# Performance work log

Measured on AMD Instinct MI355X. Metric: run time of the kernel, lower is better.

Reference implementation:

```python
import jax, jax.numpy as jnp
import numpy as np

WINDOWP = 64
LN_EPS = 1e-5


def setup_inputs() -> dict:
    key = jax.random.key(0)
    ks = jax.random.split(key, 4)
    B, T, D = 8, 2048, 1024
    feature = jax.random.normal(ks[0], (B, T, D), dtype=jnp.float32)
    wq_w = jax.random.normal(ks[1], (D, D), dtype=jnp.float32) * 0.02  # x @ wq_w + wq_b
    wq_b = jnp.zeros((D,), dtype=jnp.float32)
    w2_w = jax.random.normal(ks[2], (D,), dtype=jnp.float32) * 0.02
    w2_b = jnp.zeros((1,), dtype=jnp.float32)
    ln_g = jnp.ones((D,), dtype=jnp.float32)
    ln_b = jnp.zeros((D,), dtype=jnp.float32)
    return {"feature": feature, "wq_w": wq_w, "wq_b": wq_b,
            "w2_w": w2_w, "w2_b": w2_b, "ln_g": ln_g, "ln_b": ln_b}


def _layer_norm(y, g, b):
    mu = jnp.mean(y, axis=-1, keepdims=True)
    var = jnp.mean((y - mu) ** 2, axis=-1, keepdims=True)
    return (y - mu) * jax.lax.rsqrt(var + LN_EPS) * g + b


def reference(feature, wq_w, wq_b, w2_w, w2_b, ln_g, ln_b):
    # feature: [B, T, D]
    B, T, D = feature.shape
    W = WINDOWP
    q_local = feature @ wq_w + wq_b  # [B, T, D]

    # First W positions: v_local[:, i] = feature[:, i]
    init_buf = feature[:, :W, :]  # sliding buffer of last W outputs, [B, W, D]

    def step(buf, q_i):
        # ki = v_local[:, i-W : i+1]; slot i is still zero when read (torch writes after)
        ki = jnp.concatenate([buf, jnp.zeros((B, 1, D), feature.dtype)], axis=1)  # [B, W+1, D]
        scores = jnp.einsum('bwd,d->bw', q_i[:, None, :] * ki, w2_w) + w2_b[0]  # [B, W+1]
        alpha = jax.nn.softmax(scores, axis=1)
        v_i = jnp.einsum('bwd,bw->bd', ki, alpha)  # [B, D]
        new_buf = jnp.concatenate([buf[:, 1:, :], v_i[:, None, :]], axis=1)
        return new_buf, v_i

    qs = jnp.transpose(q_local[:, W:, :], (1, 0, 2))  # [T-W, B, D]
    _, vs = jax.lax.scan(step, init_buf, qs)          # vs: [T-W, B, D]
    v_local = jnp.concatenate([feature[:, :W, :], jnp.transpose(vs, (1, 0, 2))], axis=1)

    y = jnp.tanh(v_local) * feature + feature
    return _layer_norm(y, ln_g, ln_b)
```

## Files before the change

### kernel.cpp

```cpp
#include <hip/hip_runtime.h>
#include <hip/hip_bf16.h>

#define B_ 8
#define T_ 2048
#define D_ 1024
#define W_ 64
#define LN_EPS 1e-5f
#define LOG2E 1.4426950408889634f

typedef __attribute__((ext_vector_type(8))) short bf16x8;
typedef __attribute__((ext_vector_type(4))) float f32x4;
typedef __attribute__((ext_vector_type(2))) float f32x2;
typedef unsigned short ushort_t;

__device__ __forceinline__ ushort_t f32_to_bf16(float f) {
    union { float ff; unsigned u; } c; c.ff = f;
    unsigned r = (c.u + 0x7fffu + ((c.u >> 16) & 1u)) >> 16;
    return (ushort_t)r;
}
__device__ __forceinline__ float bf16_to_f32(ushort_t h) {
    union { unsigned u; float f; } c; c.u = ((unsigned)h) << 16; return c.f;
}
__device__ __forceinline__ float tanh_fast(float x) {
    float xx = fminf(fmaxf(x, -20.f), 20.f);
    float e = __expf(2.f * xx);
    return 1.f - 2.f / (e + 1.f);
}
__device__ __forceinline__ float readlane_f(float v, int l) {
    return __int_as_float(__builtin_amdgcn_readlane(__float_as_int(v), l));
}
template <int CTRL>
__device__ __forceinline__ float dpp_add(float x) {
    int y = __builtin_amdgcn_update_dpp(0, __float_as_int(x), CTRL, 0xf, 0xf, true);
    return x + __int_as_float(y);
}
template <int CTRL>
__device__ __forceinline__ f32x2 pk_dpp_add(f32x2 v) {
    f32x2 t;
    t.x = __int_as_float(__builtin_amdgcn_update_dpp(0, __float_as_int(v.x), CTRL, 0xf, 0xf, true));
    t.y = __int_as_float(__builtin_amdgcn_update_dpp(0, __float_as_int(v.y), CTRL, 0xf, 0xf, true));
    return v + t;
}
__device__ __forceinline__ f32x2 sum64_pair(f32x2 v) {
    v = pk_dpp_add<0x111>(v);
    v = pk_dpp_add<0x112>(v);
    v = pk_dpp_add<0x114>(v);
    v = pk_dpp_add<0x118>(v);
    v = pk_dpp_add<0x142>(v);
    v = pk_dpp_add<0x143>(v);
    return v;
}
__device__ __forceinline__ f32x2 lo2(f32x4 v) { return __builtin_shufflevector(v, v, 0, 1); }
__device__ __forceinline__ f32x2 hi2(f32x4 v) { return __builtin_shufflevector(v, v, 2, 3); }

__global__ void cvt_feat(const float* __restrict__ f, ushort_t* __restrict__ o, int n) {
    int i = blockIdx.x * blockDim.x + threadIdx.x;
    if (i < n) o[i] = f32_to_bf16(f[i]);
}

__global__ void cvt_wqT(const float* __restrict__ wq, ushort_t* __restrict__ o) {
    __shared__ float tile[64][65];
    int bi = blockIdx.x, bj = blockIdx.y, tid = threadIdx.x;
    int c = tid & 63, r4 = tid >> 6;
    for (int it = 0; it < 16; ++it) {
        int r = it * 4 + r4;
        tile[r][c] = wq[(size_t)(bi * 64 + r) * D_ + bj * 64 + c];
    }
    __syncthreads();
    for (int it = 0; it < 16; ++it) {
        int r = it * 4 + r4;
        o[(size_t)(bj * 64 + r) * D_ + bi * 64 + c] = f32_to_bf16(tile[c][r]);
    }
}

__global__ __launch_bounds__(256) void gemm_qw(
        const ushort_t* __restrict__ A, const ushort_t* __restrict__ BT,
        const float* __restrict__ wqb, const float* __restrict__ w2w,
        float* __restrict__ out) {
    const int K = 1024;
    __shared__ ushort_t Al[128][48];
    __shared__ ushort_t Bl[64][48];
    int tid = threadIdx.x;
    int lane = tid & 63, wv = tid >> 6;
    int wm = wv >> 1, wn = wv & 1;
    int m0 = blockIdx.x * 128, n0 = blockIdx.y * 64;
    int mrow = lane & 15, quad = lane >> 4;
    f32x4 acc[4][2] = {};
    for (int k0 = 0; k0 < K; k0 += 32) {
#pragma unroll
        for (int rep = 0; rep < 2; ++rep) {
            int idx = rep * 256 + tid;
            int r = idx >> 2, cp = (idx & 3) * 8;
            *(bf16x8*)&Al[r][cp] = *(const bf16x8*)&A[(size_t)(m0 + r) * K + k0 + cp];
        }
        {
            int r = tid >> 2, cp = (tid & 3) * 8;
            *(bf16x8*)&Bl[r][cp] = *(const bf16x8*)&BT[(size_t)(n0 + r) * K + k0 + cp];
        }
        __syncthreads();
        bf16x8 af[4], bfr[2];
#pragma unroll
        for (int ms = 0; ms < 4; ++ms) af[ms] = *(bf16x8*)&Al[wm * 64 + ms * 16 + mrow][quad * 8];
#pragma unroll
        for (int ns = 0; ns < 2; ++ns) bfr[ns] = *(bf16x8*)&Bl[wn * 32 + ns * 16 + mrow][quad * 8];
#pragma unroll
        for (int ms = 0; ms < 4; ++ms)
#pragma unroll
            for (int ns = 0; ns < 2; ++ns)
                acc[ms][ns] = __builtin_amdgcn_mfma_f32_16x16x32_bf16(af[ms], bfr[ns], acc[ms][ns], 0, 0, 0);
        __syncthreads();
    }
#pragma unroll
    for (int ns = 0; ns < 2; ++ns) {
        int n = n0 + wn * 32 + ns * 16 + mrow;
        float scale = w2w[n] * LOG2E, bias = wqb[n];
#pragma unroll
        for (int ms = 0; ms < 4; ++ms) {
#pragma unroll
            for (int r = 0; r < 4; ++r) {
                int m = m0 + wm * 64 + ms * 16 + quad * 4 + r;
                out[(size_t)m * D_ + n] = (acc[ms][ns][r] + bias) * scale;
            }
        }
    }
}

__global__ void featT_kernel(const float* __restrict__ feat, float* __restrict__ fT32,
                             ushort_t* __restrict__ fTh, ushort_t* __restrict__ fTl) {
    __shared__ float tile[64][65];
    int d0 = blockIdx.x * 64, b = blockIdx.y, tid = threadIdx.x;
    int c = tid & 63, r4 = tid >> 6;
#pragma unroll
    for (int it = 0; it < 16; ++it) {
        int r = it * 4 + r4;
        tile[r][c] = feat[((size_t)b * T_ + r) * D_ + d0 + c];
    }
    __syncthreads();
#pragma unroll
    for (int it = 0; it < 16; ++it) {
        int r = it * 4 + r4;
        float v = tile[c][r];
        size_t o = ((size_t)b * D_ + d0 + r) * 64 + c;
        fT32[o] = v;
        ushort_t h = f32_to_bf16(v);
        fTh[o] = h;
        fTl[o] = f32_to_bf16(v - bf16_to_f32(h));
    }
}

__global__ __launch_bounds__(256) void s0_gemm(
        const float* __restrict__ qw, const float* __restrict__ fT32,
        ushort_t* __restrict__ S0h, ushort_t* __restrict__ S0l) {
    __shared__ float As[64][17];
    __shared__ float Bs[16][65];
    int b = blockIdx.y;
    int t0 = 64 + blockIdx.x * 64;
    int tx = threadIdx.x & 15, ty = threadIdx.x >> 4;
    float acc[4][4] = {};
    for (int k0 = 0; k0 < D_; k0 += 16) {
#pragma unroll
        for (int i = 0; i < 4; ++i) {
            int idx = i * 256 + threadIdx.x;
            int r = idx >> 4, c = idx & 15;
            As[r][c] = qw[((size_t)b * T_ + t0 + r) * D_ + k0 + c];
        }
#pragma unroll
        for (int i = 0; i < 4; ++i) {
            int idx = i * 256 + threadIdx.x;
            int r = idx >> 6, c = idx & 63;
            Bs[r][c] = fT32[((size_t)b * D_ + k0 + r) * 64 + c];
        }
        __syncthreads();
#pragma unroll
        for (int kk = 0; kk < 16; ++kk)
#pragma unroll
            for (int i = 0; i < 4; ++i)
#pragma unroll
                for (int j = 0; j < 4; ++j)
                    acc[i][j] = fmaf(As[ty * 4 + i][kk], Bs[kk][tx * 4 + j], acc[i][j]);
        __syncthreads();
    }
#pragma unroll
    for (int i = 0; i < 4; ++i)
#pragma unroll
        for (int j = 0; j < 4; ++j) {
            float sc = acc[i][j];
            ushort_t h = f32_to_bf16(sc);
            size_t o = ((size_t)b * T_ + t0 + ty * 4 + i) * 64 + tx * 4 + j;
            S0h[o] = h;
            S0l[o] = f32_to_bf16(sc - bf16_to_f32(h));
        }
}

__global__ __launch_bounds__(64, 1) void core_kernel(
        const ushort_t* __restrict__ S0h, const ushort_t* __restrict__ S0l,
        float* __restrict__ gamma) {
    const int b = blockIdx.x;
    const int lane = threadIdx.x;
    const int n16 = lane & 15, quad = lane >> 4;
    __shared__ float ULDS[64 * 67];
    __shared__ __align__(16) float ALPH[64 * 68];
    __shared__ __align__(16) float B1L[16 * 68];
    __shared__ ushort_t CH[64 * 72];
    __shared__ ushort_t CL[64 * 72];
    __shared__ ushort_t CWTh[64 * 72];
    __shared__ ushort_t CWTl[64 * 72];

#pragma unroll
    for (int jj = 0; jj < 72; ++jj) {
        ushort_t idv = (jj == lane) ? (ushort_t)0x3F80 : (ushort_t)0;
        CH[lane * 72 + jj] = idv;  CL[lane * 72 + jj] = 0;
        CWTh[lane * 72 + jj] = idv; CWTl[lane * 72 + jj] = 0;
    }

#pragma unroll 1
    for (int p = 0; p < 31; ++p) {
        const int t0 = 64 + (p << 6);

        {
            bf16x8 Bh[4][2], Blo[4][2];
#pragma unroll
            for (int nt = 0; nt < 4; ++nt)
#pragma unroll
                for (int kt = 0; kt < 2; ++kt) {
                    int a = (nt * 16 + n16) * 72 + kt * 32 + quad * 8;
                    Bh[nt][kt] = *(const bf16x8*)&CH[a];
                    Blo[nt][kt] = *(const bf16x8*)&CL[a];
                }
#pragma unroll
            for (int mt = 0; mt < 4; ++mt) {
                bf16x8 Ah[2], Alo2[2];
#pragma unroll
                for (int kt = 0; kt < 2; ++kt) {
                    size_t a = ((size_t)b * T_ + t0 + mt * 16 + n16) * 64 + kt * 32 + quad * 8;
                    Ah[kt] = *(const bf16x8*)&S0h[a];
                    Alo2[kt] = *(const bf16x8*)&S0l[a];
                }
                f32x4 acc[4] = {};
#pragma unroll
                for (int nt = 0; nt < 4; ++nt)
#pragma unroll
                    for (int kt = 0; kt < 2; ++kt) {
                        acc[nt] = __builtin_amdgcn_mfma_f32_16x16x32_bf16(Ah[kt], Bh[nt][kt], acc[nt], 0, 0, 0);
                        acc[nt] = __builtin_amdgcn_mfma_f32_16x16x32_bf16(Ah[kt], Blo[nt][kt], acc[nt], 0, 0, 0);
                        acc[nt] = __builtin_amdgcn_mfma_f32_16x16x32_bf16(Alo2[kt], Bh[nt][kt], acc[nt], 0, 0, 0);
                    }
#pragma unroll
                for (int nt = 0; nt < 4; ++nt)
#pragma unroll
                    for (int r = 0; r < 4; ++r)
                        ULDS[(mt * 16 + quad * 4 + r) * 67 + nt * 16 + n16] = acc[nt][r];
            }
        }

        f32x2 Xa2[8], Xb2[8], Xc2[8], Xd2[8];
#pragma unroll
        for (int l2 = 0; l2 < 8; ++l2) {
            Xa2[l2].x = ULDS[lane * 67 + 2 * l2];
            Xa2[l2].y = ULDS[lane * 67 + 2 * l2 + 1];
            Xb2[l2].x = ULDS[lane * 67 + 16 + 2 * l2];
            Xb2[l2].y = ULDS[lane * 67 + 16 + 2 * l2 + 1];
            Xc2[l2].x = ULDS[lane * 67 + 32 + 2 * l2];
            Xc2[l2].y = ULDS[lane * 67 + 32 + 2 * l2 + 1];
            Xd2[l2].x = ULDS[lane * 67 + 48 + 2 * l2];
            Xd2[l2].y = ULDS[lane * 67 + 48 + 2 * l2 + 1];
        }
        float row = ULDS[lane];
        float nxt = ULDS[67 + lane];

#pragma unroll 1
        for (int j = 0; j < 4; ++j) {
#pragma unroll
            for (int sl = 0; sl < 16; ++sl) {
                const int s = (j << 4) | sl;
                const bool c61 = (sl <= 13);
                const bool c63 = (sl <= 14);
                bool do61 = c61 || (j < 3);
                bool do63 = c63 || (j < 3);
                float e = __builtin_amdgcn_exp2f(row);
                ALPH[s * 68 + lane] = e;
                f32x4 A[16];
                if (do63) {
#pragma unroll
                    for (int i = 0; i < 16; ++i)
                        A[i] = *(const f32x4*)&ALPH[s * 68 + i * 4];
                }
                float nxt2v = 0.f;
                if (do61) nxt2v = ULDS[(s + 2) * 67 + lane];
                f32x2 v; v.x = e; v.y = e * nxt;
                v = sum64_pair(v);
                float tot = readlane_f(v.x, 63) + 1.f;
                float cs  = readlane_f(v.y, 63);
                float r = __builtin_amdgcn_rcpf(tot);
                if (do63) {
                    float u_next = cs * r;
                    f32x2 acc0 = {0.f, 0.f}, acc1 = {0.f, 0.f}, acc2 = {0.f, 0.f}, acc3 = {0.f, 0.f};
#pragma unroll
                    for (int i2 = 0; i2 < 4; ++i2) {
                        f32x4 aa = A[i2];
                        acc0 = __builtin_elementwise_fma(lo2(aa), Xa2[2 * i2], acc0);
                        acc1 = __builtin_elementwise_fma(hi2(aa), Xa2[2 * i2 + 1], acc1);
                        f32x4 ab = A[4 + i2];
                        acc2 = __builtin_elementwise_fma(lo2(ab), Xb2[2 * i2], acc2);
                        acc3 = __builtin_elementwise_fma(hi2(ab), Xb2[2 * i2 + 1], acc3);
                        f32x4 ac = A[8 + i2];
                        acc0 = __builtin_elementwise_fma(lo2(ac), Xc2[2 * i2], acc0);
                        acc1 = __builtin_elementwise_fma(hi2(ac), Xc2[2 * i2 + 1], acc1);
                        f32x4 ad = A[12 + i2];
                        acc2 = __builtin_elementwise_fma(lo2(ad), Xd2[2 * i2], acc2);
                        acc3 = __builtin_elementwise_fma(hi2(ad), Xd2[2 * i2 + 1], acc3);
                    }
                    f32x2 u2 = (acc0 + acc1) + (acc2 + acc3);
                    float u_new = (u2.x + u2.y) * r;
                    if (j == 0)      { if (sl & 1) Xa2[sl >> 1].y = u_new; else Xa2[sl >> 1].x = u_new; }
                    else if (j == 1) { if (sl & 1) Xb2[sl >> 1].y = u_new; else Xb2[sl >> 1].x = u_new; }
                    else if (j == 2) { if (sl & 1) Xc2[sl >> 1].y = u_new; else Xc2[sl >> 1].x = u_new; }
                    else             { if (sl & 1) Xd2[sl >> 1].y = u_new; else Xd2[sl >> 1].x = u_new; }
                    if (lane > s) ULDS[lane * 67 + s] = u_new;
                    row = (lane == s) ? u_next : nxt;
                    if (do61) {
                        float pu = readlane_f(u_new, s + 2);
                        nxt = (lane == s) ? pu : nxt2v;
                    } else {
                        nxt = 0.f;
                    }
                }
                if (lane == 0) ALPH[s * 68 + 64] = r;
            }

            {
                const int J0 = j << 4;
                float rrow = ALPH[(J0 + n16) * 68 + 64];
                bf16x8 Aah[2], Aal[2];
#pragma unroll
                for (int kt = 0; kt < 2; ++kt) {
                    float v[8];
                    *(float4*)&v[0] = *(const float4*)&ALPH[(J0 + n16) * 68 + kt * 32 + quad * 8];
                    *(float4*)&v[4] = *(const float4*)&ALPH[(J0 + n16) * 68 + kt * 32 + quad * 8 + 4];
                    bf16x8 h, l;
#pragma unroll
                    for (int i = 0; i < 8; ++i) {
                        float val = v[i] * rrow;
                        ushort_t hh = f32_to_bf16(val);
                        h[i] = (short)hh;
                        l[i] = (short)f32_to_bf16(val - bf16_to_f32(hh));
                    }
                    Aah[kt] = h; Aal[kt] = l;
                }
#pragma unroll
                for (int nt = 0; nt < 4; ++nt) {
                    f32x4 a = {};
#pragma unroll
                    for (int kt = 0; kt < 2; ++kt) {
                        bf16x8 bh = *(const bf16x8*)&CWTh[(nt * 16 + n16) * 72 + kt * 32 + quad * 8];
                        bf16x8 bl = *(const bf16x8*)&CWTl[(nt * 16 + n16) * 72 + kt * 32 + quad * 8];
                        a = __builtin_amdgcn_mfma_f32_16x16x32_bf16(Aah[kt], bh, a, 0, 0, 0);
                        a = __builtin_amdgcn_mfma_f32_16x16x32_bf16(Aah[kt], bl, a, 0, 0, 0);
                        a = __builtin_amdgcn_mfma_f32_16x16x32_bf16(Aal[kt], bh, a, 0, 0, 0);
                    }
#pragma unroll
                    for (int r = 0; r < 4; ++r)
                        B1L[(quad * 4 + r) * 68 + nt * 16 + n16] = a[r];
                }
                float D[16];
#pragma unroll
                for (int sl = 0; sl < 16; ++sl) {
                    float corr = 0.f;
                    const float* arow = &ALPH[(J0 + sl) * 68 + J0];
#pragma unroll
                    for (int c = 0; c < 4; ++c) {
                        if (sl > 4 * c) {
                            float4 am = *(const float4*)&arow[4 * c];
                            if (sl > 4 * c + 0) corr = fmaf(am.x, D[4 * c + 0], corr);
                            if (sl > 4 * c + 1) corr = fmaf(am.y, D[4 * c + 1], corr);
                            if (sl > 4 * c + 2) corr = fmaf(am.z, D[4 * c + 2], corr);
                            if (sl > 4 * c + 3) corr = fmaf(am.w, D[4 * c + 3], corr);
                        }
                    }
                    float rsl = ALPH[(J0 + sl) * 68 + 64];
                    float g = fmaf(rsl, corr, B1L[sl * 68 + lane]);
                    const int slot = J0 + sl;
                    float oldv = bf16_to_f32(CH[slot * 72 + lane]) + bf16_to_f32(CL[slot * 72 + lane]);
                    D[sl] = g - oldv;
                    gamma[((size_t)b * T_ + t0 + slot) * 64 + lane] = g;
                    ushort_t gh = f32_to_bf16(g);
                    ushort_t gl2 = f32_to_bf16(g - bf16_to_f32(gh));
                    CH[slot * 72 + lane] = gh;  CL[slot * 72 + lane] = gl2;
                    CWTh[lane * 72 + slot] = gh; CWTl[lane * 72 + slot] = gl2;
                }
            }
        }
    }
}

__global__ __launch_bounds__(256) void prologue_kernel(
        const float* __restrict__ feat, float* __restrict__ out,
        const float* __restrict__ lng, const float* __restrict__ lnb) {
    int b = blockIdx.y, t = blockIdx.x, tid = threadIdx.x;
    __shared__ float red[4][2];
    size_t base = ((size_t)b * T_ + t) * D_;
    float4 f4 = *(const float4*)&feat[base + tid * 4];
    float4 y;
    y.x = tanh_fast(f4.x) * f4.x + f4.x;
    y.y = tanh_fast(f4.y) * f4.y + f4.y;
    y.z = tanh_fast(f4.z) * f4.z + f4.z;
    y.w = tanh_fast(f4.w) * f4.w + f4.w;
    float s1 = y.x + y.y + y.z + y.w;
    float s2 = y.x * y.x + y.y * y.y + y.z * y.z + y.w * y.w;
#pragma unroll
    for (int m = 1; m < 64; m <<= 1) { s1 += __shfl_xor(s1, m, 64); s2 += __shfl_xor(s2, m, 64); }
    if ((tid & 63) == 0) { red[tid >> 6][0] = s1; red[tid >> 6][1] = s2; }
    __syncthreads();
    float mu = (red[0][0] + red[1][0] + red[2][0] + red[3][0]) * (1.f / D_);
    float m2 = (red[0][1] + red[1][1] + red[2][1] + red[3][1]) * (1.f / D_);
    float rv = rsqrtf(fmaxf(m2 - mu * mu, 0.f) + LN_EPS);
    float4 g4 = *(const float4*)&lng[tid * 4];
    float4 b4 = *(const float4*)&lnb[tid * 4];
    float4 o;
    o.x = (y.x - mu) * rv * g4.x + b4.x;
    o.y = (y.y - mu) * rv * g4.y + b4.y;
    o.z = (y.z - mu) * rv * g4.z + b4.z;
    o.w = (y.w - mu) * rv * g4.w + b4.w;
    *(float4*)&out[base + tid * 4] = o;
}

__global__ __launch_bounds__(256) void final_kernel(
        const float* __restrict__ gamma, const ushort_t* __restrict__ fTh,
        const ushort_t* __restrict__ fTl, const float* __restrict__ feat,
        const float* __restrict__ lng, const float* __restrict__ lnb,
        float* __restrict__ out) {
    const int b = blockIdx.y;
    const int t0 = 64 + blockIdx.x * 16;
    const int tid = threadIdx.x, lane = tid & 63, wv = tid >> 6;
    const int n16 = lane & 15, quad = lane >> 4;
    __shared__ float wsum[4][16][2];
    __shared__ float lnp[16][2];

    bf16x8 Ah[2], Alo[2];
    {
        const float* gr = &gamma[((size_t)b * T_ + t0 + n16) * 64];
#pragma unroll
        for (int kt = 0; kt < 2; ++kt) {
            float g[8];
            *(float4*)&g[0] = *(const float4*)&gr[kt * 32 + quad * 8];
            *(float4*)&g[4] = *(const float4*)&gr[kt * 32 + quad * 8 + 4];
            bf16x8 h, l;
#pragma unroll
            for (int i = 0; i < 8; ++i) {
                ushort_t hh = f32_to_bf16(g[i]);
                h[i] = (short)hh;
                l[i] = (short)f32_to_bf16(g[i] - bf16_to_f32(hh));
            }
            Ah[kt] = h; Alo[kt] = l;
        }
    }
    f32x4 acc[16];
#pragma unroll
    for (int j = 0; j < 16; ++j) {
        const int d = wv * 256 + j * 16 + n16;
        const ushort_t* fr = &fTh[((size_t)b * D_ + d) * 64];
        const ushort_t* fr2 = &fTl[((size_t)b * D_ + d) * 64];
        f32x4 a = {0.f, 0.f, 0.f, 0.f};
#pragma unroll
        for (int kt = 0; kt < 2; ++kt) {
            bf16x8 bh = *(const bf16x8*)&fr[kt * 32 + quad * 8];
            bf16x8 bl = *(const bf16x8*)&fr2[kt * 32 + quad * 8];
            a = __builtin_amdgcn_mfma_f32_16x16x32_bf16(Ah[kt], bh, a, 0, 0, 0);
            a = __builtin_amdgcn_mfma_f32_16x16x32_bf16(Ah[kt], bl, a, 0, 0, 0);
            a = __builtin_amdgcn_mfma_f32_16x16x32_bf16(Alo[kt], bh, a, 0, 0, 0);
        }
        acc[j] = a;
    }
    float s1[4] = {0.f, 0.f, 0.f, 0.f}, s2[4] = {0.f, 0.f, 0.f, 0.f};
#pragma unroll
    for (int j = 0; j < 16; ++j) {
        const int d = wv * 256 + j * 16 + n16;
#pragma unroll
        for (int r = 0; r < 4; ++r) {
            float f = feat[((size_t)b * T_ + t0 + quad * 4 + r) * D_ + d];
            float y = tanh_fast(acc[j][r]) * f + f;
            acc[j][r] = y;
            s1[r] += y;
            s2[r] += y * y;
        }
    }
#pragma unroll
    for (int m = 1; m < 16; m <<= 1)
#pragma unroll
        for (int r = 0; r < 4; ++r) { s1[r] += __shfl_xor(s1[r], m, 64); s2[r] += __shfl_xor(s2[r], m, 64); }
    if (n16 == 0) {
#pragma unroll
        for (int r = 0; r < 4; ++r) { wsum[wv][quad * 4 + r][0] = s1[r]; wsum[wv][quad * 4 + r][1] = s2[r]; }
    }
    __syncthreads();
    if (tid < 16) {
        float a = 0.f, c = 0.f;
#pragma unroll
        for (int w2 = 0; w2 < 4; ++w2) { a += wsum[w2][tid][0]; c += wsum[w2][tid][1]; }
        float mu = a * (1.f / D_);
        float var = c * (1.f / D_) - mu * mu;
        lnp[tid][0] = mu;
        lnp[tid][1] = rsqrtf(fmaxf(var, 0.f) + LN_EPS);
    }
    __syncthreads();
#pragma unroll
    for (int j = 0; j < 16; ++j) {
        const int d = wv * 256 + j * 16 + n16;
        float gd = lng[d], bd = lnb[d];
#pragma unroll
        for (int r = 0; r < 4; ++r) {
            int row = quad * 4 + r;
            out[((size_t)b * T_ + t0 + row) * D_ + d] = (acc[j][r] - lnp[row][0]) * lnp[row][1] * gd + bd;
        }
    }
}

extern "C" void kernel_launch(void* const* d_in, const int* in_sizes, int n_in,
                              void* d_out, int out_size, void* d_ws, size_t ws_size,
                              hipStream_t stream) {
    const float* feature = (const float*)d_in[0];
    const float* wq_w    = (const float*)d_in[1];
    const float* wq_b    = (const float*)d_in[2];
    const float* w2_w    = (const float*)d_in[3];
    const float* ln_g    = (const float*)d_in[5];
    const float* ln_b    = (const float*)d_in[6];
    float* out = (float*)d_out;

    uint8_t* ws = (uint8_t*)d_ws;
    ushort_t* featbf = (ushort_t*)(ws);
    ushort_t* wqT    = (ushort_t*)(ws + 32u * 1024 * 1024);
    float*    gamma = (float*)(ws);
    ushort_t* S0h   = (ushort_t*)(ws + 4u * 1024 * 1024);
    ushort_t* S0l   = (ushort_t*)(ws + 6u * 1024 * 1024);
    float*    fT32  = (float*)(ws + 8u * 1024 * 1024);
    ushort_t* fTh   = (ushort_t*)(ws + 10u * 1024 * 1024);
    ushort_t* fTl   = (ushort_t*)(ws + 11u * 1024 * 1024);

    const int ntot = B_ * T_ * D_;
    cvt_feat<<<(ntot + 255) / 256, 256, 0, stream>>>(feature, featbf, ntot);
    cvt_wqT<<<dim3(16, 16), 256, 0, stream>>>(wq_w, wqT);
    gemm_qw<<<dim3(128, 16), 256, 0, stream>>>(featbf, wqT, wq_b, w2_w, out);
    featT_kernel<<<dim3(16, 8), 256, 0, stream>>>(feature, fT32, fTh, fTl);
    s0_gemm<<<dim3(31, 8), 256, 0, stream>>>(out, fT32, S0h, S0l);
    core_kernel<<<8, 64, 0, stream>>>(S0h, S0l, gamma);
    prologue_kernel<<<dim3(64, 8), 256, 0, stream>>>(feature, out, ln_g, ln_b);
    final_kernel<<<dim3(124, 8), 256, 0, stream>>>(gamma, fTh, fTl, feature, ln_g, ln_b, out);
}
```

Before: 1.373 ms.

## Use split-bf16 MFMA for score GEMM and merge prep/prologue kernels

Replaces the fp32 FMA tiled s0_gemm with a three-product split-bf16 MFMA formulation that reads a new bf16 hi/lo copy of the first 64 feature rows produced in featT_kernel. Merges feature conversion and weight transpose into one launch, and folds the prologue LayerNorm blocks into final_kernel as extra blocks. Aims to cut the compute cost of the score GEMM and launch overhead, at the risk of slight precision change from the split-bf16 approximation.

After: 1.336 ms. 1.03x faster.

```diff
diff --git a/kernel.cpp b/kernel.cpp
--- a/kernel.cpp
+++ b/kernel.cpp
@@ -53,23 +53,30 @@
 __device__ __forceinline__ f32x2 lo2(f32x4 v) { return __builtin_shufflevector(v, v, 0, 1); }
 __device__ __forceinline__ f32x2 hi2(f32x4 v) { return __builtin_shufflevector(v, v, 2, 3); }
 
-__global__ void cvt_feat(const float* __restrict__ f, ushort_t* __restrict__ o, int n) {
-    int i = blockIdx.x * blockDim.x + threadIdx.x;
-    if (i < n) o[i] = f32_to_bf16(f[i]);
-}
-
-__global__ void cvt_wqT(const float* __restrict__ wq, ushort_t* __restrict__ o) {
+__global__ void prep_kernel(const float* __restrict__ f, ushort_t* __restrict__ o,
+                            const float* __restrict__ wq, ushort_t* __restrict__ wqT) {
     __shared__ float tile[64][65];
-    int bi = blockIdx.x, bj = blockIdx.y, tid = threadIdx.x;
-    int c = tid & 63, r4 = tid >> 6;
-    for (int it = 0; it < 16; ++it) {
-        int r = it * 4 + r4;
-        tile[r][c] = wq[(size_t)(bi * 64 + r) * D_ + bj * 64 + c];
-    }
-    __syncthreads();
-    for (int it = 0; it < 16; ++it) {
-        int r = it * 4 + r4;
-        o[(size_t)(bj * 64 + r) * D_ + bi * 64 + c] = f32_to_bf16(tile[c][r]);
+    int tid = threadIdx.x;
+    if (blockIdx.x < 32768) {
+        int i = blockIdx.x * 512 + tid * 2;
+        float2 v = *(const float2*)&f[i];
+        ushort2 w;
+        w.x = f32_to_bf16(v.x);
+        w.y = f32_to_bf16(v.y);
+        *(ushort2*)&o[i] = w;
+    } else {
+        int bid = blockIdx.x - 32768;
+        int bi = bid & 15, bj = bid >> 4;
+        int c = tid & 63, r4 = tid >> 6;
+        for (int it = 0; it < 16; ++it) {
+            int r = it * 4 + r4;
+            tile[r][c] = wq[(size_t)(bi * 64 + r) * D_ + bj * 64 + c];
+        }
+        __syncthreads();
+        for (int it = 0; it < 16; ++it) {
+            int r = it * 4 + r4;
+            wqT[(size_t)(bj * 64 + r) * D_ + bi * 64 + c] = f32_to_bf16(tile[c][r]);
+        }
     }
 }
 
@@ -125,15 +132,21 @@
     }
 }
 
-__global__ void featT_kernel(const float* __restrict__ feat, float* __restrict__ fT32,
-                             ushort_t* __restrict__ fTh, ushort_t* __restrict__ fTl) {
+__global__ void featT_kernel(const float* __restrict__ feat,
+                             ushort_t* __restrict__ fTh, ushort_t* __restrict__ fTl,
+                             ushort_t* __restrict__ f0h, ushort_t* __restrict__ f0l) {
     __shared__ float tile[64][65];
     int d0 = blockIdx.x * 64, b = blockIdx.y, tid = threadIdx.x;
     int c = tid & 63, r4 = tid >> 6;
 #pragma unroll
     for (int it = 0; it < 16; ++it) {
         int r = it * 4 + r4;
-        tile[r][c] = feat[((size_t)b * T_ + r) * D_ + d0 + c];
+        float v = feat[((size_t)b * T_ + r) * D_ + d0 + c];
+        tile[r][c] = v;
+        ushort_t h = f32_to_bf16(v);
+        size_t o0 = ((size_t)b * 64 + r) * D_ + d0 + c;
+        f0h[o0] = h;
+        f0l[o0] = f32_to_bf16(v - bf16_to_f32(h));
     }
     __syncthreads();
 #pragma unroll
@@ -141,7 +154,6 @@
         int r = it * 4 + r4;
         float v = tile[c][r];
         size_t o = ((size_t)b * D_ + d0 + r) * 64 + c;
-        fT32[o] = v;
         ushort_t h = f32_to_bf16(v);
         fTh[o] = h;
         fTl[o] = f32_to_bf16(v - bf16_to_f32(h));
@@ -149,46 +161,46 @@
 }
 
 __global__ __launch_bounds__(256) void s0_gemm(
-        const float* __restrict__ qw, const float* __restrict__ fT32,
+        const float* __restrict__ qw, const ushort_t* __restrict__ f0h,
+        const ushort_t* __restrict__ f0l,
         ushort_t* __restrict__ S0h, ushort_t* __restrict__ S0l) {
-    __shared__ float As[64][17];
-    __shared__ float Bs[16][65];
-    int b = blockIdx.y;
-    int t0 = 64 + blockIdx.x * 64;
-    int tx = threadIdx.x & 15, ty = threadIdx.x >> 4;
-    float acc[4][4] = {};
-    for (int k0 = 0; k0 < D_; k0 += 16) {
-#pragma unroll
-        for (int i = 0; i < 4; ++i) {
-            int idx = i * 256 + threadIdx.x;
-            int r = idx >> 4, c = idx & 15;
-            As[r][c] = qw[((size_t)b * T_ + t0 + r) * D_ + k0 + c];
-        }
-#pragma unroll
-        for (int i = 0; i < 4; ++i) {
-            int idx = i * 256 + threadIdx.x;
-            int r = idx >> 6, c = idx & 63;
-            Bs[r][c] = fT32[((size_t)b * D_ + k0 + r) * 64 + c];
-        }
-        __syncthreads();
-#pragma unroll
-        for (int kk = 0; kk < 16; ++kk)
-#pragma unroll
-            for (int i = 0; i < 4; ++i)
-#pragma unroll
-                for (int j = 0; j < 4; ++j)
-                    acc[i][j] = fmaf(As[ty * 4 + i][kk], Bs[kk][tx * 4 + j], acc[i][j]);
-        __syncthreads();
-    }
-#pragma unroll
-    for (int i = 0; i < 4; ++i)
-#pragma unroll
-        for (int j = 0; j < 4; ++j) {
-            float sc = acc[i][j];
+    const int b = blockIdx.y;
+    const int t0 = 64 + blockIdx.x * 64;
+    const int tid = threadIdx.x, lane = tid & 63, wv = tid >> 6;
+    const int n16 = lane & 15, quad = lane >> 4;
+    const float* qrow = &qw[((size_t)b * T_ + t0 + wv * 16 + n16) * D_];
+    f32x4 acc[4] = {};
+#pragma unroll 4
+    for (int k0 = 0; k0 < D_; k0 += 32) {
+        float a8[8];
+        *(float4*)&a8[0] = *(const float4*)&qrow[k0 + quad * 8];
+        *(float4*)&a8[4] = *(const float4*)&qrow[k0 + quad * 8 + 4];
+        bf16x8 ah, al;
+#pragma unroll
+        for (int i = 0; i < 8; ++i) {
+            ushort_t hh = f32_to_bf16(a8[i]);
+            ah[i] = (short)hh;
+            al[i] = (short)f32_to_bf16(a8[i] - bf16_to_f32(hh));
+        }
+#pragma unroll
+        for (int nt = 0; nt < 4; ++nt) {
+            const size_t fo = ((size_t)b * 64 + nt * 16 + n16) * D_ + k0 + quad * 8;
+            bf16x8 bh = *(const bf16x8*)&f0h[fo];
+            bf16x8 bl = *(const bf16x8*)&f0l[fo];
+            acc[nt] = __builtin_amdgcn_mfma_f32_16x16x32_bf16(ah, bh, acc[nt], 0, 0, 0);
+            acc[nt] = __builtin_amdgcn_mfma_f32_16x16x32_bf16(ah, bl, acc[nt], 0, 0, 0);
+            acc[nt] = __builtin_amdgcn_mfma_f32_16x16x32_bf16(al, bh, acc[nt], 0, 0, 0);
+        }
+    }
+#pragma unroll
+    for (int nt = 0; nt < 4; ++nt)
+#pragma unroll
+        for (int r = 0; r < 4; ++r) {
+            float sc = acc[nt][r];
             ushort_t h = f32_to_bf16(sc);
-            size_t o = ((size_t)b * T_ + t0 + ty * 4 + i) * 64 + tx * 4 + j;
-            S0h[o] = h;
-            S0l[o] = f32_to_bf16(sc - bf16_to_f32(h));
+            size_t o2 = ((size_t)b * T_ + t0 + wv * 16 + quad * 4 + r) * 64 + nt * 16 + n16;
+            S0h[o2] = h;
+            S0l[o2] = f32_to_bf16(sc - bf16_to_f32(h));
         }
 }
 
@@ -393,48 +405,49 @@
     }
 }
 
-__global__ __launch_bounds__(256) void prologue_kernel(
-        const float* __restrict__ feat, float* __restrict__ out,
-        const float* __restrict__ lng, const float* __restrict__ lnb) {
-    int b = blockIdx.y, t = blockIdx.x, tid = threadIdx.x;
-    __shared__ float red[4][2];
-    size_t base = ((size_t)b * T_ + t) * D_;
-    float4 f4 = *(const float4*)&feat[base + tid * 4];
-    float4 y;
-    y.x = tanh_fast(f4.x) * f4.x + f4.x;
-    y.y = tanh_fast(f4.y) * f4.y + f4.y;
-    y.z = tanh_fast(f4.z) * f4.z + f4.z;
-    y.w = tanh_fast(f4.w) * f4.w + f4.w;
-    float s1 = y.x + y.y + y.z + y.w;
-    float s2 = y.x * y.x + y.y * y.y + y.z * y.z + y.w * y.w;
-#pragma unroll
-    for (int m = 1; m < 64; m <<= 1) { s1 += __shfl_xor(s1, m, 64); s2 += __shfl_xor(s2, m, 64); }
-    if ((tid & 63) == 0) { red[tid >> 6][0] = s1; red[tid >> 6][1] = s2; }
-    __syncthreads();
-    float mu = (red[0][0] + red[1][0] + red[2][0] + red[3][0]) * (1.f / D_);
-    float m2 = (red[0][1] + red[1][1] + red[2][1] + red[3][1]) * (1.f / D_);
-    float rv = rsqrtf(fmaxf(m2 - mu * mu, 0.f) + LN_EPS);
-    float4 g4 = *(const float4*)&lng[tid * 4];
-    float4 b4 = *(const float4*)&lnb[tid * 4];
-    float4 o;
-    o.x = (y.x - mu) * rv * g4.x + b4.x;
-    o.y = (y.y - mu) * rv * g4.y + b4.y;
-    o.z = (y.z - mu) * rv * g4.z + b4.z;
-    o.w = (y.w - mu) * rv * g4.w + b4.w;
-    *(float4*)&out[base + tid * 4] = o;
-}
-
 __global__ __launch_bounds__(256) void final_kernel(
         const float* __restrict__ gamma, const ushort_t* __restrict__ fTh,
         const ushort_t* __restrict__ fTl, const float* __restrict__ feat,
         const float* __restrict__ lng, const float* __restrict__ lnb,
         float* __restrict__ out) {
     const int b = blockIdx.y;
-    const int t0 = 64 + blockIdx.x * 16;
-    const int tid = threadIdx.x, lane = tid & 63, wv = tid >> 6;
-    const int n16 = lane & 15, quad = lane >> 4;
+    const int tid = threadIdx.x;
     __shared__ float wsum[4][16][2];
     __shared__ float lnp[16][2];
+    __shared__ float red[4][2];
+
+    if (blockIdx.x >= 124) {
+        int t = blockIdx.x - 124;
+        size_t base = ((size_t)b * T_ + t) * D_;
+        float4 f4 = *(const float4*)&feat[base + tid * 4];
+        float4 y;
+        y.x = tanh_fast(f4.x) * f4.x + f4.x;
+        y.y = tanh_fast(f4.y) * f4.y + f4.y;
+        y.z = tanh_fast(f4.z) * f4.z + f4.z;
+        y.w = tanh_fast(f4.w) * f4.w + f4.w;
+        float s1 = y.x + y.y + y.z + y.w;
+        float s2 = y.x * y.x + y.y * y.y + y.z * y.z + y.w * y.w;
+#pragma unroll
+        for (int m = 1; m < 64; m <<= 1) { s1 += __shfl_xor(s1, m, 64); s2 += __shfl_xor(s2, m, 64); }
+        if ((tid & 63) == 0) { red[tid >> 6][0] = s1; red[tid >> 6][1] = s2; }
+        __syncthreads();
+        float mu = (red[0][0] + red[1][0] + red[2][0] + red[3][0]) * (1.f / D_);
+        float m2 = (red[0][1] + red[1][1] + red[2][1] + red[3][1]) * (1.f / D_);
+        float rv = rsqrtf(fmaxf(m2 - mu * mu, 0.f) + LN_EPS);
+        float4 g4 = *(const float4*)&lng[tid * 4];
+        float4 b4 = *(const float4*)&lnb[tid * 4];
+        float4 o;
+        o.x = (y.x - mu) * rv * g4.x + b4.x;
+        o.y = (y.y - mu) * rv * g4.y + b4.y;
+        o.z = (y.z - mu) * rv * g4.z + b4.z;
+        o.w = (y.w - mu) * rv * g4.w + b4.w;
+        *(float4*)&out[base + tid * 4] = o;
+        return;
+    }
+
+    const int t0 = 64 + blockIdx.x * 16;
+    const int lane = tid & 63, wv = tid >> 6;
+    const int n16 = lane & 15, quad = lane >> 4;
 
     bf16x8 Ah[2], Alo[2];
     {
@@ -532,17 +545,15 @@
     float*    gamma = (float*)(ws);
     ushort_t* S0h   = (ushort_t*)(ws + 4u * 1024 * 1024);
     ushort_t* S0l   = (ushort_t*)(ws + 6u * 1024 * 1024);
-    float*    fT32  = (float*)(ws + 8u * 1024 * 1024);
-    ushort_t* fTh   = (ushort_t*)(ws + 10u * 1024 * 1024);
-    ushort_t* fTl   = (ushort_t*)(ws + 11u * 1024 * 1024);
-
-    const int ntot = B_ * T_ * D_;
-    cvt_feat<<<(ntot + 255) / 256, 256, 0, stream>>>(feature, featbf, ntot);
-    cvt_wqT<<<dim3(16, 16), 256, 0, stream>>>(wq_w, wqT);
+    ushort_t* fTh   = (ushort_t*)(ws + 8u * 1024 * 1024);
+    ushort_t* fTl   = (ushort_t*)(ws + 9u * 1024 * 1024);
+    ushort_t* f0h   = (ushort_t*)(ws + 10u * 1024 * 1024);
+    ushort_t* f0l   = (ushort_t*)(ws + 11u * 1024 * 1024);
+
+    prep_kernel<<<33024, 256, 0, stream>>>(feature, featbf, wq_w, wqT);
     gemm_qw<<<dim3(128, 16), 256, 0, stream>>>(featbf, wqT, wq_b, w2_w, out);
-    featT_kernel<<<dim3(16, 8), 256, 0, stream>>>(feature, fT32, fTh, fTl);
-    s0_gemm<<<dim3(31, 8), 256, 0, stream>>>(out, fT32, S0h, S0l);
+    featT_kernel<<<dim3(16, 8), 256, 0, stream>>>(feature, fTh, fTl, f0h, f0l);
+    s0_gemm<<<dim3(31, 8), 256, 0, stream>>>(out, f0h, f0l, S0h, S0l);
     core_kernel<<<8, 64, 0, stream>>>(S0h, S0l, gamma);
-    prologue_kernel<<<dim3(64, 8), 256, 0, stream>>>(feature, out, ln_g, ln_b);
-    final_kernel<<<dim3(124, 8), 256, 0, stream>>>(gamma, fTh, fTl, feature, ln_g, ln_b, out);
-}
+    final_kernel<<<dim3(188, 8), 256, 0, stream>>>(gamma, fTh, fTl, feature, ln_g, ln_b, out);
+}
```
